# Kernel tuning notes

Measured on AMD Instinct MI355X. Metric: run time of the kernel, lower is better.

The kernel has to match this reference:

```python
import jax, jax.numpy as jnp
import numpy as np

HEADS = 8
DIM_HEAD = 64

def setup_inputs() -> dict:
    key = jax.random.key(0)
    k1, k2, k3 = jax.random.split(key, 3)
    B, L, D = 8, 4096, 512
    hidden = HEADS * DIM_HEAD  # 512
    x = jax.random.normal(k1, (B, L, D), dtype=jnp.float32)
    # Conv1d(kernel_size=1) weights, squeezed to 2D matrices
    Wqkv = jax.random.normal(k2, (3 * hidden, D), dtype=jnp.float32) * (1.0 / np.sqrt(D))
    Wout = jax.random.normal(k3, (D, hidden), dtype=jnp.float32) * (1.0 / np.sqrt(hidden))
    bout = jnp.zeros((D,), dtype=jnp.float32)
    return {"x": x, "Wqkv": Wqkv, "Wout": Wout, "bout": bout}

def reference(x, Wqkv, Wout, bout):
    B, L, D = x.shape
    H, C = HEADS, DIM_HEAD
    # pointwise conv == linear over channel dim: (b, 3*H*C, l)
    qkv = jnp.einsum('bld,od->bol', x, Wqkv)
    qkv = qkv.reshape(B, 3, H, C, L)  # channel split order: (qkv, heads, c)
    q, k, v = qkv[:, 0], qkv[:, 1], qkv[:, 2]  # each (b, h, c, l)
    k = jax.nn.softmax(k, axis=-1)   # softmax over sequence
    q = jax.nn.softmax(q, axis=-2)   # softmax over feature dim (q_norm=True)
    context = jnp.einsum('bhdn,bhen->bhde', k, v)   # (b,h,c,c)
    out = jnp.einsum('bhde,bhdn->bhen', context, q)  # (b,h,c,l)
    out = out.reshape(B, H * C, L)
    y = jnp.einsum('bcl,dc->bld', out, Wout) + bout  # to_out + permute back
    return y
```

## Files before the change

### kernel.cpp

```cpp
#include <hip/hip_runtime.h>

#define L 4096
#define D 512
#define NCH 16

typedef __bf16 bf16x8 __attribute__((ext_vector_type(8)));
typedef float  f32x4  __attribute__((ext_vector_type(4)));

__device__ __forceinline__ void load_lds16(const void* g, void* l) {
    __builtin_amdgcn_global_load_lds(
        (const __attribute__((address_space(1))) void*)g,
        (__attribute__((address_space(3))) void*)l, 16, 0, 0);
}

#define NX8  (8 * 4096 * 512 / 8)
#define NW18 (1536 * 512 / 8)
#define NW28 (512 * 512 / 8)
__global__ __launch_bounds__(256) void convert_all(const float* __restrict__ x,
                                                   const float* __restrict__ Wq,
                                                   const float* __restrict__ Wo,
                                                   __bf16* __restrict__ dst) {
    int i = blockIdx.x * 256 + threadIdx.x;
    if (i >= NX8 + NW18 + NW28) return;
    const float* s;
    if (i < NX8)             s = x  + (size_t)i * 8;
    else if (i < NX8 + NW18) s = Wq + (size_t)(i - NX8) * 8;
    else                     s = Wo + (size_t)(i - NX8 - NW18) * 8;
    float4 a = ((const float4*)s)[0], b = ((const float4*)s)[1];
    bf16x8 o = {(__bf16)a.x, (__bf16)a.y, (__bf16)a.z, (__bf16)a.w,
                (__bf16)b.x, (__bf16)b.y, (__bf16)b.z, (__bf16)b.w};
    *(bf16x8*)(dst + (size_t)i * 8) = o;
}

template <int M, int N, int K, typename CT>
__global__ __launch_bounds__(256) void gemm_bf16_mfma(
    const __bf16* __restrict__ A, size_t aStride,
    const __bf16* __restrict__ B, size_t bStride,
    CT* __restrict__ C, size_t cStride,
    const float* __restrict__ bias) {
    __shared__ __align__(16) __bf16 sA[128 * 64];
    __shared__ __align__(16) __bf16 sB[128 * 64];
    const int b  = blockIdx.z;
    const int m0 = blockIdx.y * 128;
    const int n0 = blockIdx.x * 128;
    const int t    = threadIdx.x;
    const int wave = t >> 6, lane = t & 63;
    const int wm = (wave & 1) * 64, wn = (wave >> 1) * 64;
    const __bf16* Ab = A + (size_t)b * aStride;
    const __bf16* Bb = B + (size_t)b * bStride;
    CT* Cb = C + (size_t)b * cStride;

    f32x4 acc[4][4];
#pragma unroll
    for (int i = 0; i < 4; i++)
#pragma unroll
        for (int j = 0; j < 4; j++) acc[i][j] = (f32x4)(0.0f);

    const int fr = lane & 15;
    const int g  = lane >> 4;

    for (int k0 = 0; k0 < K; k0 += 64) {
        __syncthreads();
#pragma unroll
        for (int c = 0; c < 4; c++) {
            const int idx = c * 256 + t;
            const int row = idx >> 3, cc = idx & 7;
            const int scc = cc ^ (row & 7);
            load_lds16(Ab + (size_t)(m0 + row) * K + k0 + scc * 8, &sA[idx * 8]);
            load_lds16(Bb + (size_t)(n0 + row) * K + k0 + scc * 8, &sB[idx * 8]);
        }
        __syncthreads();
#pragma unroll
        for (int kh = 0; kh < 2; kh++) {
            const int ko = ((kh * 4 + g) ^ (fr & 7)) * 8;
            bf16x8 af[4], bfr[4];
#pragma unroll
            for (int i = 0; i < 4; i++) {
                af[i]  = *(const bf16x8*)&sA[(wm + i * 16 + fr) * 64 + ko];
                bfr[i] = *(const bf16x8*)&sB[(wn + i * 16 + fr) * 64 + ko];
            }
#pragma unroll
            for (int i = 0; i < 4; i++)
#pragma unroll
                for (int j = 0; j < 4; j++)
                    acc[i][j] = __builtin_amdgcn_mfma_f32_16x16x32_bf16(af[i], bfr[j], acc[i][j], 0, 0, 0);
        }
    }

    const int col = lane & 15, rbase = g * 4;
#pragma unroll
    for (int j = 0; j < 4; j++) {
        const int n = n0 + wn + j * 16 + col;
        const float bv = bias ? bias[n] : 0.0f;
#pragma unroll
        for (int i = 0; i < 4; i++) {
#pragma unroll
            for (int r = 0; r < 4; r++) {
                const int m = m0 + wm + i * 16 + rbase + r;
                Cb[(size_t)m * N + n] = (CT)(acc[i][j][r] + bv);
            }
        }
    }
}

__global__ __launch_bounds__(256) void kstats(const __bf16* __restrict__ qkv,
                                              float2* __restrict__ stats) {
    const int r = blockIdx.x;
    const int b = r >> 9, hc = r & 511;
    const __bf16* row = qkv + (size_t)b * 1536 * L + (size_t)(512 + hc) * L;
    __shared__ float sred[4];
    const int t = threadIdx.x;
    const bf16x8* p = (const bf16x8*)row;
    bf16x8 c0 = p[t * 2], c1 = p[t * 2 + 1];
    float v[16];
    float m = -1e30f;
#pragma unroll
    for (int j = 0; j < 8; j++) {
        v[j] = (float)c0[j];
        v[8 + j] = (float)c1[j];
    }
#pragma unroll
    for (int j = 0; j < 16; j++) m = fmaxf(m, v[j]);
#pragma unroll
    for (int off = 32; off > 0; off >>= 1) m = fmaxf(m, __shfl_down(m, off, 64));
    if ((t & 63) == 0) sred[t >> 6] = m;
    __syncthreads();
    const float m4 = fmaxf(fmaxf(sred[0], sred[1]), fmaxf(sred[2], sred[3]));
    float s = 0.f;
#pragma unroll
    for (int j = 0; j < 16; j++) s += __expf(v[j] - m4);
#pragma unroll
    for (int off = 32; off > 0; off >>= 1) s += __shfl_down(s, off, 64);
    __syncthreads();
    if ((t & 63) == 0) sred[t >> 6] = s;
    __syncthreads();
    if (t == 0) {
        const float stot = sred[0] + sred[1] + sred[2] + sred[3];
        stats[r] = make_float2(m4, 1.0f / stot);
    }
}

#define SKS 264
__global__ __launch_bounds__(256) void context_mfma(const __bf16* __restrict__ qkv,
                                                    const float2* __restrict__ stats,
                                                    float* __restrict__ ctxp) {
    __shared__ __align__(16) __bf16 smem[2 * 64 * SKS];
    __shared__ float smax[64];
    __bf16* sk = smem;
    __bf16* sv = smem + 64 * SKS;
    const int chunk = blockIdx.x;
    const int bh = blockIdx.y;
    const int b = bh >> 3, h = bh & 7;
    const __bf16* kbase = qkv + (size_t)b * 1536 * L + (size_t)(512 + h * 64) * L;
    const __bf16* vbase = qkv + (size_t)b * 1536 * L + (size_t)(1024 + h * 64) * L;
    const int t = threadIdx.x;
    if (t < 64) smax[t] = stats[bh * 64 + t].x;
    __syncthreads();

    {
        const int d = t >> 2, noff = (t & 3) * 64;
        const int n0 = chunk * 256;
        const __bf16* kp = kbase + (size_t)d * L + n0 + noff;
        const __bf16* vp = vbase + (size_t)d * L + n0 + noff;
        const float md = smax[d];
#pragma unroll
        for (int c = 0; c < 8; c++) {
            bf16x8 kk = *(const bf16x8*)(kp + c * 8);
            bf16x8 vv = *(const bf16x8*)(vp + c * 8);
            bf16x8 ek;
#pragma unroll
            for (int j = 0; j < 8; j++) ek[j] = (__bf16)__expf((float)kk[j] - md);
            *(bf16x8*)&sk[d * SKS + noff + c * 8] = ek;
            *(bf16x8*)&sv[d * SKS + noff + c * 8] = vv;
        }
    }
    __syncthreads();

    const int wave = t >> 6, lane = t & 63;
    const int fr = lane & 15, kq = (lane >> 4) * 8;
    f32x4 acc[4][4];
#pragma unroll
    for (int i = 0; i < 4; i++)
#pragma unroll
        for (int j = 0; j < 4; j++) acc[i][j] = (f32x4)(0.0f);
#pragma unroll
    for (int kh = 0; kh < 2; kh++) {
        const int koff = wave * 64 + kh * 32 + kq;
        bf16x8 af[4], bfr[4];
#pragma unroll
        for (int i = 0; i < 4; i++) {
            af[i]  = *(const bf16x8*)&sk[(i * 16 + fr) * SKS + koff];
            bfr[i] = *(const bf16x8*)&sv[(i * 16 + fr) * SKS + koff];
        }
#pragma unroll
        for (int i = 0; i < 4; i++)
#pragma unroll
            for (int j = 0; j < 4; j++)
                acc[i][j] = __builtin_amdgcn_mfma_f32_16x16x32_bf16(af[i], bfr[j], acc[i][j], 0, 0, 0);
    }
    __syncthreads();

    float* red = (float*)smem;
    const int col = lane & 15, rbase = (lane >> 4) * 4;
#pragma unroll
    for (int i = 0; i < 4; i++)
#pragma unroll
        for (int j = 0; j < 4; j++)
#pragma unroll
            for (int r = 0; r < 4; r++) {
                const int dd = i * 16 + rbase + r;
                const int ee = j * 16 + col;
                red[wave * 4096 + dd * 64 + ee] = acc[i][j][r];
            }
    __syncthreads();
    float* cp = ctxp + ((size_t)chunk * 64 + bh) * 4096;
#pragma unroll
    for (int gg = 0; gg < 4; gg++) {
        const int idx = t * 16 + gg * 4;
        f32x4 s = *(const f32x4*)&red[idx];
        s += *(const f32x4*)&red[4096 + idx];
        s += *(const f32x4*)&red[8192 + idx];
        s += *(const f32x4*)&red[12288 + idx];
        *(f32x4*)&cp[idx] = s;
    }
}

__global__ __launch_bounds__(256) void ctx_reduce(const float* __restrict__ ctxp,
                                                  const float2* __restrict__ stats,
                                                  __bf16* __restrict__ ctxT) {
    const int bh = blockIdx.x >> 2, quarter = blockIdx.x & 3;
    const int t = threadIdx.x;
    const int flat = quarter * 1024 + t * 4;
    const int d = flat >> 6, e0 = flat & 63;
    f32x4 s = (f32x4)(0.0f);
    for (int ch = 0; ch < NCH; ch++)
        s += *(const f32x4*)&ctxp[((size_t)ch * 64 + bh) * 4096 + flat];
    const float inv = stats[bh * 64 + d].y;
    __bf16* o = ctxT + (size_t)bh * 4096;
#pragma unroll
    for (int j = 0; j < 4; j++) o[(e0 + j) * 64 + d] = (__bf16)(s[j] * inv);
}

#define SPS 66
__global__ __launch_bounds__(256) void pv_fused(__bf16* __restrict__ qkv,
                                                const __bf16* __restrict__ ctxT) {
    __shared__ __align__(16) __bf16 sp[256 * SPS];
    __shared__ __align__(16) __bf16 sctx[64 * SPS];
    __shared__ float sinv[256];
    const int tileN = blockIdx.x;
    const int bh = blockIdx.y;
    const int b = bh >> 3, h = bh & 7;
    const int t = threadIdx.x;
    const int n0 = tileN * 256;
    const __bf16* qbase = qkv + (size_t)b * 1536 * L + (size_t)(h * 64) * L;

    {
        const int e = t >> 2, c = t & 3;
        const bf16x8* src = (const bf16x8*)(ctxT + ((size_t)bh * 64 + e) * 64 + c * 16);
        *(bf16x8*)&sctx[e * SPS + c * 16] = src[0];
        *(bf16x8*)&sctx[e * SPS + c * 16 + 8] = src[1];
    }

    float m = -1e30f;
    float qv[64];
#pragma unroll
    for (int d = 0; d < 64; d++) {
        qv[d] = (float)qbase[(size_t)d * L + n0 + t];
        m = fmaxf(m, qv[d]);
    }
    float s = 0.f;
#pragma unroll
    for (int d0 = 0; d0 < 64; d0 += 8) {
        bf16x8 ek;
#pragma unroll
        for (int j = 0; j < 8; j++) {
            float e = __expf(qv[d0 + j] - m);
            s += e;
            ek[j] = (__bf16)e;
        }
        *(bf16x8*)&sp[t * SPS + d0] = ek;
    }
    sinv[t] = 1.0f / s;
    __syncthreads();

    const int wave = t >> 6, lane = t & 63;
    const int wm = wave * 64;
    const int fr = lane & 15, kq = (lane >> 4) * 8;
    f32x4 acc[4][4];
#pragma unroll
    for (int i = 0; i < 4; i++)
#pragma unroll
        for (int j = 0; j < 4; j++) acc[i][j] = (f32x4)(0.0f);
#pragma unroll
    for (int kh = 0; kh < 2; kh++) {
        bf16x8 af[4], bfr[4];
#pragma unroll
        for (int i = 0; i < 4; i++)
            af[i] = *(const bf16x8*)&sp[(wm + i * 16 + fr) * SPS + kh * 32 + kq];
#pragma unroll
        for (int j = 0; j < 4; j++)
            bfr[j] = *(const bf16x8*)&sctx[(j * 16 + fr) * SPS + kh * 32 + kq];
#pragma unroll
        for (int i = 0; i < 4; i++)
#pragma unroll
            for (int j = 0; j < 4; j++)
                acc[i][j] = __builtin_amdgcn_mfma_f32_16x16x32_bf16(af[i], bfr[j], acc[i][j], 0, 0, 0);
    }

    __bf16* ob = qkv + (size_t)b * 1536 * L + (size_t)512 * L;
    const int col = lane & 15, rbase = (lane >> 4) * 4;
#pragma unroll
    for (int i = 0; i < 4; i++) {
#pragma unroll
        for (int r = 0; r < 4; r++) {
            const int nl = wm + i * 16 + rbase + r;
            const float inv = sinv[nl];
            const size_t rowoff = (size_t)(n0 + nl) * 512 + h * 64;
#pragma unroll
            for (int j = 0; j < 4; j++)
                ob[rowoff + j * 16 + col] = (__bf16)(acc[i][j][r] * inv);
        }
    }
}

extern "C" void kernel_launch(void* const* d_in, const int* in_sizes, int n_in,
                              void* d_out, int out_size, void* d_ws, size_t ws_size,
                              hipStream_t stream) {
    const float* x    = (const float*)d_in[0];
    const float* Wqkv = (const float*)d_in[1];
    const float* Wout = (const float*)d_in[2];
    const float* bout = (const float*)d_in[3];
    float* y = (float*)d_out;

    __bf16* qkv   = (__bf16*)d_ws;
    float*  ctxp  = (float*)(qkv + (size_t)8 * 1536 * L);
    __bf16* xb    = (__bf16*)(ctxp + (size_t)NCH * 64 * 4096);
    __bf16* Wqb   = xb + (size_t)8 * 4096 * 512;
    __bf16* Wob   = Wqb + (size_t)1536 * 512;
    float2* stats = (float2*)(Wob + (size_t)512 * 512);
    __bf16* ctxT  = (__bf16*)(stats + 4096);

    const int convBlocks = (NX8 + NW18 + NW28 + 255) / 256;
    convert_all<<<dim3(convBlocks), 256, 0, stream>>>(x, Wqkv, Wout, xb);

    gemm_bf16_mfma<1536, 4096, 512, __bf16><<<dim3(4096 / 128, 1536 / 128, 8), 256, 0, stream>>>(
        Wqb, 0, xb, (size_t)4096 * 512, qkv, (size_t)1536 * 4096, nullptr);

    kstats<<<dim3(4096), 256, 0, stream>>>(qkv, stats);
    context_mfma<<<dim3(NCH, 64), 256, 0, stream>>>(qkv, stats, ctxp);
    ctx_reduce<<<dim3(256), 256, 0, stream>>>(ctxp, stats, ctxT);
    pv_fused<<<dim3(L / 256, 64), 256, 0, stream>>>(qkv, ctxT);

    const __bf16* outT = qkv + (size_t)512 * L;
    gemm_bf16_mfma<4096, 512, 512, float><<<dim3(512 / 128, 4096 / 128, 8), 256, 0, stream>>>(
        outT, (size_t)1536 * L, Wob, 0, y, (size_t)4096 * 512, bout);
}
```

Before: 284.8 us.

## Fuse x fp32-to-bf16 conversion into QKV GEMM and shrink K-tile to 32

Removes the standalone conversion of x to bf16 by having the QKV GEMM load fp32 x directly, convert in registers and store to LDS. Weights are still converted by a smaller kernel. Both GEMMs now use a 32-wide K tile with a matching swizzle, which halves LDS use but doubles the number of barriers per K. The fused path loads B through registers instead of async global-to-LDS loads, and each x element is reread and reconverted by all 12 M-tile blocks.

```diff
diff --git a/kernel.cpp b/kernel.cpp
--- a/kernel.cpp
+++ b/kernel.cpp
@@ -13,23 +13,86 @@
         (__attribute__((address_space(3))) void*)l, 16, 0, 0);
 }
 
-#define NX8  (8 * 4096 * 512 / 8)
 #define NW18 (1536 * 512 / 8)
 #define NW28 (512 * 512 / 8)
-__global__ __launch_bounds__(256) void convert_all(const float* __restrict__ x,
-                                                   const float* __restrict__ Wq,
-                                                   const float* __restrict__ Wo,
-                                                   __bf16* __restrict__ dst) {
+__global__ __launch_bounds__(256) void convert_w(const float* __restrict__ Wq,
+                                                 const float* __restrict__ Wo,
+                                                 __bf16* __restrict__ dst) {
     int i = blockIdx.x * 256 + threadIdx.x;
-    if (i >= NX8 + NW18 + NW28) return;
-    const float* s;
-    if (i < NX8)             s = x  + (size_t)i * 8;
-    else if (i < NX8 + NW18) s = Wq + (size_t)(i - NX8) * 8;
-    else                     s = Wo + (size_t)(i - NX8 - NW18) * 8;
+    if (i >= NW18 + NW28) return;
+    const float* s = (i < NW18) ? Wq + (size_t)i * 8 : Wo + (size_t)(i - NW18) * 8;
     float4 a = ((const float4*)s)[0], b = ((const float4*)s)[1];
     bf16x8 o = {(__bf16)a.x, (__bf16)a.y, (__bf16)a.z, (__bf16)a.w,
                 (__bf16)b.x, (__bf16)b.y, (__bf16)b.z, (__bf16)b.w};
     *(bf16x8*)(dst + (size_t)i * 8) = o;
+}
+
+__global__ __launch_bounds__(256) void qkv_gemm_xf32(
+    const __bf16* __restrict__ Wq,
+    const float* __restrict__ x,
+    __bf16* __restrict__ qkv) {
+    __shared__ __align__(16) __bf16 sA[128 * 32];
+    __shared__ __align__(16) __bf16 sB[128 * 32];
+    const int b  = blockIdx.z;
+    const int m0 = blockIdx.y * 128;
+    const int n0 = blockIdx.x * 128;
+    const int t    = threadIdx.x;
+    const int wave = t >> 6, lane = t & 63;
+    const int wm = (wave & 1) * 64, wn = (wave >> 1) * 64;
+    const float* xb = x + (size_t)b * L * D;
+    __bf16* Cb = qkv + (size_t)b * 1536 * L;
+
+    f32x4 acc[4][4];
+#pragma unroll
+    for (int i = 0; i < 4; i++)
+#pragma unroll
+        for (int j = 0; j < 4; j++) acc[i][j] = (f32x4)(0.0f);
+
+    const int fr = lane & 15;
+    const int cq = lane >> 4;
+    const int ko = (cq ^ ((fr >> 1) & 3)) * 8;
+
+    for (int k0 = 0; k0 < D; k0 += 32) {
+        __syncthreads();
+#pragma unroll
+        for (int c = 0; c < 2; c++) {
+            const int idx = c * 256 + t;
+            const int row = idx >> 2, cc = idx & 3;
+            const int scc = cc ^ ((row >> 1) & 3);
+            load_lds16(Wq + (size_t)(m0 + row) * D + k0 + scc * 8, &sA[idx * 8]);
+            const float4* src = (const float4*)(xb + (size_t)(n0 + row) * D + k0 + scc * 8);
+            float4 lo = src[0], hi = src[1];
+            bf16x8 o = {(__bf16)lo.x, (__bf16)lo.y, (__bf16)lo.z, (__bf16)lo.w,
+                        (__bf16)hi.x, (__bf16)hi.y, (__bf16)hi.z, (__bf16)hi.w};
+            *(bf16x8*)&sB[idx * 8] = o;
+        }
+        __syncthreads();
+        bf16x8 af[4], bfr[4];
+#pragma unroll
+        for (int i = 0; i < 4; i++) {
+            af[i]  = *(const bf16x8*)&sA[(wm + i * 16 + fr) * 32 + ko];
+            bfr[i] = *(const bf16x8*)&sB[(wn + i * 16 + fr) * 32 + ko];
+        }
+#pragma unroll
+        for (int i = 0; i < 4; i++)
+#pragma unroll
+            for (int j = 0; j < 4; j++)
+                acc[i][j] = __builtin_amdgcn_mfma_f32_16x16x32_bf16(af[i], bfr[j], acc[i][j], 0, 0, 0);
+    }
+
+    const int col = lane & 15, rbase = (lane >> 4) * 4;
+#pragma unroll
+    for (int j = 0; j < 4; j++) {
+        const int n = n0 + wn + j * 16 + col;
+#pragma unroll
+        for (int i = 0; i < 4; i++) {
+#pragma unroll
+            for (int r = 0; r < 4; r++) {
+                const int m = m0 + wm + i * 16 + rbase + r;
+                Cb[(size_t)m * L + n] = (__bf16)acc[i][j][r];
+            }
+        }
+    }
 }
 
 template <int M, int N, int K, typename CT>
@@ -38,8 +101,8 @@
     const __bf16* __restrict__ B, size_t bStride,
     CT* __restrict__ C, size_t cStride,
     const float* __restrict__ bias) {
-    __shared__ __align__(16) __bf16 sA[128 * 64];
-    __shared__ __align__(16) __bf16 sB[128 * 64];
+    __shared__ __align__(16) __bf16 sA[128 * 32];
+    __shared__ __align__(16) __bf16 sB[128 * 32];
     const int b  = blockIdx.z;
     const int m0 = blockIdx.y * 128;
     const int n0 = blockIdx.x * 128;
@@ -57,37 +120,34 @@
         for (int j = 0; j < 4; j++) acc[i][j] = (f32x4)(0.0f);
 
     const int fr = lane & 15;
-    const int g  = lane >> 4;
-
-    for (int k0 = 0; k0 < K; k0 += 64) {
+    const int cq = lane >> 4;
+    const int ko = (cq ^ ((fr >> 1) & 3)) * 8;
+
+    for (int k0 = 0; k0 < K; k0 += 32) {
         __syncthreads();
 #pragma unroll
-        for (int c = 0; c < 4; c++) {
+        for (int c = 0; c < 2; c++) {
             const int idx = c * 256 + t;
-            const int row = idx >> 3, cc = idx & 7;
-            const int scc = cc ^ (row & 7);
+            const int row = idx >> 2, cc = idx & 3;
+            const int scc = cc ^ ((row >> 1) & 3);
             load_lds16(Ab + (size_t)(m0 + row) * K + k0 + scc * 8, &sA[idx * 8]);
             load_lds16(Bb + (size_t)(n0 + row) * K + k0 + scc * 8, &sB[idx * 8]);
         }
         __syncthreads();
-#pragma unroll
-        for (int kh = 0; kh < 2; kh++) {
-            const int ko = ((kh * 4 + g) ^ (fr & 7)) * 8;
-            bf16x8 af[4], bfr[4];
-#pragma unroll
-            for (int i = 0; i < 4; i++) {
-                af[i]  = *(const bf16x8*)&sA[(wm + i * 16 + fr) * 64 + ko];
-                bfr[i] = *(const bf16x8*)&sB[(wn + i * 16 + fr) * 64 + ko];
-            }
-#pragma unroll
-            for (int i = 0; i < 4; i++)
-#pragma unroll
-                for (int j = 0; j < 4; j++)
-                    acc[i][j] = __builtin_amdgcn_mfma_f32_16x16x32_bf16(af[i], bfr[j], acc[i][j], 0, 0, 0);
-        }
-    }
-
-    const int col = lane & 15, rbase = g * 4;
+        bf16x8 af[4], bfr[4];
+#pragma unroll
+        for (int i = 0; i < 4; i++) {
+            af[i]  = *(const bf16x8*)&sA[(wm + i * 16 + fr) * 32 + ko];
+            bfr[i] = *(const bf16x8*)&sB[(wn + i * 16 + fr) * 32 + ko];
+        }
+#pragma unroll
+        for (int i = 0; i < 4; i++)
+#pragma unroll
+            for (int j = 0; j < 4; j++)
+                acc[i][j] = __builtin_amdgcn_mfma_f32_16x16x32_bf16(af[i], bfr[j], acc[i][j], 0, 0, 0);
+    }
+
+    const int col = lane & 15, rbase = (lane >> 4) * 4;
 #pragma unroll
     for (int j = 0; j < 4; j++) {
         const int n = n0 + wn + j * 16 + col;
@@ -334,17 +394,14 @@
 
     __bf16* qkv   = (__bf16*)d_ws;
     float*  ctxp  = (float*)(qkv + (size_t)8 * 1536 * L);
-    __bf16* xb    = (__bf16*)(ctxp + (size_t)NCH * 64 * 4096);
-    __bf16* Wqb   = xb + (size_t)8 * 4096 * 512;
+    __bf16* Wqb   = (__bf16*)(ctxp + (size_t)NCH * 64 * 4096);
     __bf16* Wob   = Wqb + (size_t)1536 * 512;
     float2* stats = (float2*)(Wob + (size_t)512 * 512);
     __bf16* ctxT  = (__bf16*)(stats + 4096);
 
-    const int convBlocks = (NX8 + NW18 + NW28 + 255) / 256;
-    convert_all<<<dim3(convBlocks), 256, 0, stream>>>(x, Wqkv, Wout, xb);
-
-    gemm_bf16_mfma<1536, 4096, 512, __bf16><<<dim3(4096 / 128, 1536 / 128, 8), 256, 0, stream>>>(
-        Wqb, 0, xb, (size_t)4096 * 512, qkv, (size_t)1536 * 4096, nullptr);
+    convert_w<<<dim3((NW18 + NW28 + 255) / 256), 256, 0, stream>>>(Wqkv, Wout, Wqb);
+
+    qkv_gemm_xf32<<<dim3(4096 / 128, 1536 / 128, 8), 256, 0, stream>>>(Wqb, x, qkv);
 
     kstats<<<dim3(4096), 256, 0, stream>>>(qkv, stats);
     context_mfma<<<dim3(NCH, 64), 256, 0, stream>>>(qkv, stats, ctxp);
```

Result: slower. 311.3 us (+9.3%).
